# Performance work log

Hardware: AMD Instinct MI355X
Metric: run time of the kernel (lower is better)

The kernel has to match this reference:

```python
import jax, jax.numpy as jnp
import numpy as np

NEG_SLOPE = 0.01  # nn.LeakyReLU default


def gcn_conv(x, src, dst, deg_inv_sqrt, W, b, n_nodes):
    """PyG GCNConv with self-loops already folded into (src, dst, deg_inv_sqrt).
    out = scatter_add(norm_e * (x @ W)[src]) + b, norm_e = d_src^-1/2 * d_dst^-1/2."""
    h = x @ W  # [N, F_out] -- transform first (F_out < F_in saves gather traffic)
    norm = (deg_inv_sqrt[src] * deg_inv_sqrt[dst])[:, None]  # [E, 1]
    msg = h[src] * norm  # [E, F_out]
    return jax.ops.segment_sum(msg, dst, num_segments=n_nodes) + b


def setup_inputs() -> dict:
    key = jax.random.key(0)
    ks = jax.random.split(key, 8)
    N, E, F_IN, F_HID, F_OUT = 50000, 800000, 256, 128, 64
    x = jax.random.normal(ks[0], (N, F_IN), dtype=jnp.float32)
    edge_index = jax.random.randint(ks[1], (2, E), 0, N, dtype=jnp.int64)
    def glorot(k, shape):
        lim = float(np.sqrt(6.0 / (shape[0] + shape[1])))
        return jax.random.uniform(k, shape, jnp.float32, -lim, lim)
    return {
        "x": x,
        "edge_index": edge_index,
        "W1": glorot(ks[2], (F_IN, F_HID)),
        "b1": jnp.zeros((F_HID,), jnp.float32),
        "W_mu": glorot(ks[3], (F_HID, F_OUT)),
        "b_mu": jnp.zeros((F_OUT,), jnp.float32),
        "W_logvar": glorot(ks[4], (F_HID, F_OUT)),
        "b_logvar": jnp.zeros((F_OUT,), jnp.float32),
    }


def reference(x, edge_index, W1, b1, W_mu, b_mu, W_logvar, b_logvar):
    n_nodes = x.shape[0]
    loops = jnp.arange(n_nodes, dtype=edge_index.dtype)
    src = jnp.concatenate([edge_index[0], loops])
    dst = jnp.concatenate([edge_index[1], loops])
    # degree on destination nodes (includes self-loop); >= 1 so rsqrt is safe
    deg = jax.ops.segment_sum(jnp.ones_like(dst, dtype=x.dtype), dst, num_segments=n_nodes)
    deg_inv_sqrt = jax.lax.rsqrt(deg)

    h = gcn_conv(x, src, dst, deg_inv_sqrt, W1, b1, n_nodes)
    h = jax.nn.leaky_relu(h, NEG_SLOPE)
    mu = gcn_conv(h, src, dst, deg_inv_sqrt, W_mu, b_mu, n_nodes)
    logvar = gcn_conv(h, src, dst, deg_inv_sqrt, W_logvar, b_logvar, n_nodes)
    return (mu, logvar)
```

## Files before the change

### kernel.cpp

```cpp
#include <hip/hip_runtime.h>

#define NEG_SLOPE 0.01f
#define EPB 4096
#define NB_SHIFT 8

typedef __attribute__((ext_vector_type(8))) short bf16x8;
typedef __attribute__((ext_vector_type(4))) float floatx4;

__device__ __forceinline__ short f2bf(float f) {
    union { float f; unsigned u; } v; v.f = f;
    unsigned u = v.u;
    u += 0x7FFF + ((u >> 16) & 1);
    return (short)(u >> 16);
}
__device__ __forceinline__ float bf2f(short s) {
    union { unsigned u; float f; } v;
    v.u = ((unsigned)(unsigned short)s) << 16;
    return v.f;
}


__launch_bounds__(256)
__global__ void hist_pack(const int* __restrict__ dst, int E, int B, int K,
                          int* __restrict__ btot,
                          const float* __restrict__ W1, const float* __restrict__ Wmu,
                          const float* __restrict__ Wlv,
                          short* __restrict__ w1f, short* __restrict__ wcatf) {
    __shared__ int lh[256];
    int bid = blockIdx.x;
    int tid = threadIdx.x;
    if (bid < B) {
        lh[tid] = 0;
        __syncthreads();
        int lo = bid * EPB, hi = min(lo + EPB, E);
        for (int e = lo + tid; e < hi; e += 256)
            atomicAdd(&lh[dst[e] >> NB_SHIFT], 1);
        __syncthreads();
        int v = lh[tid];
        if (v) atomicAdd(&btot[tid], v);
    } else {
        int i = (bid - B) * 256 + tid;
        if (i < 128 * 256) {
            int j  = i & 7;
            int ln = (i >> 3) & 15;
            int q  = (i >> 7) & 3;
            int t  = (i >> 9) & 7;
            int kb = i >> 12;
            int n = t * 16 + ln;
            int k = kb * 32 + q * 8 + j;
            w1f[i] = f2bf(W1[k * 128 + n]);
        } else {
            int i2 = i - 128 * 256;
            int j  = i2 & 7;
            int ln = (i2 >> 3) & 15;
            int q  = (i2 >> 7) & 3;
            int t  = (i2 >> 9) & 7;
            int kb = i2 >> 12;
            int n = t * 16 + ln;
            int k = kb * 32 + q * 8 + j;
            wcatf[i2] = f2bf((n < 64) ? Wmu[k * 64 + n] : Wlv[k * 64 + (n - 64)]);
        }
    }
}

__global__ void bucket_scan(const int* __restrict__ btot, int K, int E,
                            int* __restrict__ bstart, int* __restrict__ bcur) {
    __shared__ int waveTot[4];
    __shared__ int waveOff[4];
    int tid = threadIdx.x;
    int lane = tid & 63, wave = tid >> 6;
    int v = (tid < K) ? btot[tid] : 0;
    int s = v;
    #pragma unroll
    for (int o = 1; o < 64; o <<= 1) {
        int t = __shfl_up(s, o);
        if (lane >= o) s += t;
    }
    if (lane == 63) waveTot[wave] = s;
    __syncthreads();
    if (tid == 0) {
        int acc = 0;
        #pragma unroll
        for (int w = 0; w < 4; w++) { waveOff[w] = acc; acc += waveTot[w]; }
    }
    __syncthreads();
    int excl = s - v + waveOff[wave];
    if (tid < K) { bstart[tid] = excl; bcur[tid] = excl; }
    if (tid == 0) bstart[K] = E;
}

template<int K>
__device__ __forceinline__ void gemm1_body(int blk, int tid, const float* __restrict__ Ap,
                                           const short* __restrict__ Bfrag,
                                           short* __restrict__ C, int M) {
    int w = tid >> 6;
    int lane = tid & 63;
    int ln = lane & 15;
    int q  = lane >> 4;
    int rowTile = blk * 128 + w * 32;

    int r0 = rowTile + ln;
    int r1 = rowTile + 16 + ln;
    int r0c = (r0 < M) ? r0 : (M - 1);
    int r1c = (r1 < M) ? r1 : (M - 1);

    const float* a0F = Ap + (size_t)r0c * K + q * 8;
    const float* a1F = Ap + (size_t)r1c * K + q * 8;
    const short* bLane = Bfrag + lane * 8;

    floatx4 acc[2][8];
    #pragma unroll
    for (int f = 0; f < 2; f++)
        #pragma unroll
        for (int t = 0; t < 8; t++) acc[f][t] = (floatx4){0.f, 0.f, 0.f, 0.f};

    constexpr int NIT = K / 32;
    #pragma unroll
    for (int kb = 0; kb < NIT; kb++) {
        int kt = kb * 32;
        bf16x8 aF0, aF1;
        float4 x0 = *(const float4*)(a0F + kt);
        float4 x1 = *(const float4*)(a0F + kt + 4);
        float4 y0 = *(const float4*)(a1F + kt);
        float4 y1 = *(const float4*)(a1F + kt + 4);
        aF0[0] = f2bf(x0.x); aF0[1] = f2bf(x0.y); aF0[2] = f2bf(x0.z); aF0[3] = f2bf(x0.w);
        aF0[4] = f2bf(x1.x); aF0[5] = f2bf(x1.y); aF0[6] = f2bf(x1.z); aF0[7] = f2bf(x1.w);
        aF1[0] = f2bf(y0.x); aF1[1] = f2bf(y0.y); aF1[2] = f2bf(y0.z); aF1[3] = f2bf(y0.w);
        aF1[4] = f2bf(y1.x); aF1[5] = f2bf(y1.y); aF1[6] = f2bf(y1.z); aF1[7] = f2bf(y1.w);
        bf16x8 bF[8];
        #pragma unroll
        for (int t = 0; t < 8; t++)
            bF[t] = *(const bf16x8*)(bLane + (size_t)(kb * 8 + t) * 512);
        #pragma unroll
        for (int t = 0; t < 8; t++) {
            acc[0][t] = __builtin_amdgcn_mfma_f32_16x16x32_bf16(aF0, bF[t], acc[0][t], 0, 0, 0);
            acc[1][t] = __builtin_amdgcn_mfma_f32_16x16x32_bf16(aF1, bF[t], acc[1][t], 0, 0, 0);
        }
    }

    #pragma unroll
    for (int f = 0; f < 2; f++) {
        #pragma unroll
        for (int reg = 0; reg < 4; reg++) {
            int r = rowTile + f * 16 + q * 4 + reg;
            if (r < M) {
                #pragma unroll
                for (int t = 0; t < 8; t++)
                    C[(size_t)r * 128 + t * 16 + ln] = f2bf(acc[f][t][reg]);
            }
        }
    }
}

__launch_bounds__(256)
__global__ void scatter_gemm1(const int* __restrict__ src, const int* __restrict__ dst,
                              int E, int B, int* __restrict__ bcur,
                              unsigned* __restrict__ bucketed,
                              const float* __restrict__ x, const short* __restrict__ w1f,
                              short* __restrict__ z1, int M) {
    __shared__ int lh[256];
    __shared__ int lofs[256];
    __shared__ int gbase[256];
    __shared__ unsigned srt[EPB];
    __shared__ int waveTot[4];
    __shared__ int waveOff[4];
    int bid = blockIdx.x;
    int tid = threadIdx.x;
    if (bid < B) {
        lh[tid] = 0;
        __syncthreads();
        int lo = bid * EPB, hi = min(lo + EPB, E);
        for (int e = lo + tid; e < hi; e += 256)
            atomicAdd(&lh[dst[e] >> NB_SHIFT], 1);
        __syncthreads();
        int v = lh[tid];
        int lane = tid & 63, wave = tid >> 6;
        int s = v;
        #pragma unroll
        for (int o = 1; o < 64; o <<= 1) {
            int t = __shfl_up(s, o);
            if (lane >= o) s += t;
        }
        if (lane == 63) waveTot[wave] = s;
        __syncthreads();
        if (tid == 0) {
            int acc = 0;
            #pragma unroll
            for (int w = 0; w < 4; w++) { waveOff[w] = acc; acc += waveTot[w]; }
        }
        __syncthreads();
        int excl = s - v + waveOff[wave];
        lofs[tid] = excl;
        if (v) gbase[tid] = atomicAdd(&bcur[tid], v);
        __syncthreads();
        lh[tid] = excl;
        __syncthreads();
        for (int e = lo + tid; e < hi; e += 256) {
            int d = dst[e];
            unsigned rec = (unsigned)(src[e] & 0xFFFF) | ((unsigned)d << 16);
            int p = atomicAdd(&lh[d >> NB_SHIFT], 1);
            srt[p] = rec;
        }
        __syncthreads();
        int cnt = hi - lo;
        for (int p = tid; p < cnt; p += 256) {
            unsigned r = srt[p];
            int k = r >> 24;
            bucketed[gbase[k] + (p - lofs[k])] = r;
        }
    } else {
        gemm1_body<256>(bid - B, tid, x, w1f, z1, M);
    }
}

__global__ void fill_csr_deg(const unsigned* __restrict__ bucketed,
                             const int* __restrict__ bstart,
                             int* __restrict__ row_ptr, int* __restrict__ row_end,
                             float* __restrict__ dis,
                             unsigned short* __restrict__ csr_src, int N) {
    __shared__ int cnt[256];
    __shared__ int rp[256];
    __shared__ int waveTot[4];
    __shared__ int waveOff[4];
    __shared__ unsigned short lcsr[8192];
    int k = blockIdx.x;
    int tid = threadIdx.x;
    int base = k << NB_SHIFT;
    cnt[tid] = 0;
    __syncthreads();
    int lo = bstart[k], hi = bstart[k + 1];
    int m = hi - lo;
    for (int e = lo + tid; e < hi; e += 256)
        atomicAdd(&cnt[(bucketed[e] >> 16) & 255], 1);
    __syncthreads();
    int v = cnt[tid];
    int lane = tid & 63, wave = tid >> 6;
    int s = v;
    #pragma unroll
    for (int o = 1; o < 64; o <<= 1) {
        int t = __shfl_up(s, o);
        if (lane >= o) s += t;
    }
    if (lane == 63) waveTot[wave] = s;
    __syncthreads();
    if (tid == 0) {
        int acc = 0;
        #pragma unroll
        for (int w = 0; w < 4; w++) { waveOff[w] = acc; acc += waveTot[w]; }
    }
    __syncthreads();
    int excl = s - v + waveOff[wave];
    rp[tid] = excl;
    int node = base + tid;
    if (node < N) {
        row_ptr[node] = lo + excl;
        row_end[node] = lo + excl + v;
        dis[node] = rsqrtf(1.0f + (float)v);
    }
    __syncthreads();
    if (m <= 8192) {
        for (int e = lo + tid; e < hi; e += 256) {
            unsigned sd = bucketed[e];
            int p = atomicAdd(&rp[(sd >> 16) & 255], 1);
            lcsr[p] = (unsigned short)(sd & 0xFFFFu);
        }
        __syncthreads();
        for (int i = tid; i < m; i += 256) csr_src[lo + i] = lcsr[i];
    } else {
        for (int e = lo + tid; e < hi; e += 256) {
            unsigned sd = bucketed[e];
            int p = atomicAdd(&rp[(sd >> 16) & 255], 1);
            csr_src[lo + p] = (unsigned short)(sd & 0xFFFFu);
        }
    }
}


__launch_bounds__(256)
__global__ void agg1_gemm2(const short* __restrict__ z1, const int* __restrict__ row_ptr,
                           const int* __restrict__ row_end,
                           const unsigned short* __restrict__ csr_src,
                           const float* __restrict__ dis, const float* __restrict__ b1,
                           const short* __restrict__ wcatf,
                           short* __restrict__ z2, int N) {
    __shared__ short htile[64 * 128];
    int tid = threadIdx.x;
    int w = tid >> 6;
    int lane = tid & 63;
    int qi = lane >> 4;
    int fl = lane & 15;
    int fo = fl * 8;
    int base = blockIdx.x * 64;

    const short* zb = z1 + fo;
    for (int i = 0; i < 16; ++i) {
        int local = w * 16 + i;
        int node = base + local;
        int swz = ((local & 7) * 8);
        short* hrow = &htile[(local * 128 + fo) ^ swz];
        if (node < N) {
            int start = row_ptr[node], end = row_end[node];
            float acc[8];
            #pragma unroll
            for (int t = 0; t < 8; t++) acc[t] = 0.f;
            for (int bse = start; bse < end; bse += 64) {
                int n = end - bse; n = (n > 64) ? 64 : n;
                int idx = (int)csr_src[bse + ((lane < n) ? lane : 0)];
                float dl = dis[idx];
                for (int j = 0; j < n; j += 8) {
                    int j0 = j + qi;
                    int j1 = j0 + 4;
                    int c0 = (j0 < n) ? j0 : 0;
                    int c1 = (j1 < n) ? j1 : 0;
                    int s0 = __shfl(idx, c0);
                    int s1 = __shfl(idx, c1);
                    float d0 = __shfl(dl, c0);
                    float d1 = __shfl(dl, c1);
                    if (j0 >= n) d0 = 0.f;
                    if (j1 >= n) d1 = 0.f;
                    bf16x8 zv0 = *(const bf16x8*)(zb + (size_t)s0 * 128);
                    bf16x8 zv1 = *(const bf16x8*)(zb + (size_t)s1 * 128);
                    #pragma unroll
                    for (int t = 0; t < 8; t++)
                        acc[t] = fmaf(d0, bf2f(zv0[t]), fmaf(d1, bf2f(zv1[t]), acc[t]));
                }
            }
            if (qi == 0) {
                float dn = dis[node];
                bf16x8 zs = *(const bf16x8*)(zb + (size_t)node * 128);
                #pragma unroll
                for (int t = 0; t < 8; t++) acc[t] = fmaf(dn, bf2f(zs[t]), acc[t]);
            }
            #pragma unroll
            for (int t = 0; t < 8; t++) {
                acc[t] += __shfl_xor(acc[t], 16);
                acc[t] += __shfl_xor(acc[t], 32);
            }
            if (qi == 0) {
                float d = dis[node];
                bf16x8 ov;
                #pragma unroll
                for (int t = 0; t < 8; t++) {
                    float v = fmaf(d, acc[t], b1[fo + t]);
                    v = (v > 0.f) ? v : NEG_SLOPE * v;
                    ov[t] = f2bf(v);
                }
                *(bf16x8*)hrow = ov;
            }
        } else if (qi == 0) {
            *(bf16x8*)hrow = (bf16x8){0, 0, 0, 0, 0, 0, 0, 0};
        }
    }
    __syncthreads();

    int rw = (w & 1) * 32;
    int tc = (w >> 1) * 4;
    int ln = fl;
    int q  = qi;
    int r0 = rw + ln;
    int r1 = rw + 16 + ln;
    const short* bLane = wcatf + lane * 8;

    floatx4 acc[2][4];
    #pragma unroll
    for (int f = 0; f < 2; f++)
        #pragma unroll
        for (int t = 0; t < 4; t++) acc[f][t] = (floatx4){0.f, 0.f, 0.f, 0.f};

    #pragma unroll
    for (int kb = 0; kb < 4; kb++) {
        int k0 = kb * 32 + q * 8;
        bf16x8 aF0 = *(const bf16x8*)&htile[(r0 * 128 + k0) ^ ((r0 & 7) * 8)];
        bf16x8 aF1 = *(const bf16x8*)&htile[(r1 * 128 + k0) ^ ((r1 & 7) * 8)];
        bf16x8 bF[4];
        #pragma unroll
        for (int t = 0; t < 4; t++)
            bF[t] = *(const bf16x8*)(bLane + (size_t)(kb * 8 + tc + t) * 512);
        #pragma unroll
        for (int t = 0; t < 4; t++) {
            acc[0][t] = __builtin_amdgcn_mfma_f32_16x16x32_bf16(aF0, bF[t], acc[0][t], 0, 0, 0);
            acc[1][t] = __builtin_amdgcn_mfma_f32_16x16x32_bf16(aF1, bF[t], acc[1][t], 0, 0, 0);
        }
    }

    #pragma unroll
    for (int f = 0; f < 2; f++) {
        #pragma unroll
        for (int reg = 0; reg < 4; reg++) {
            int gr = base + rw + f * 16 + q * 4 + reg;
            if (gr < N) {
                float s = dis[gr];
                #pragma unroll
                for (int t = 0; t < 4; t++)
                    z2[(size_t)gr * 128 + (tc + t) * 16 + ln] = f2bf(s * acc[f][t][reg]);
            }
        }
    }
}

__launch_bounds__(256)
__global__ void agg_layer2(const short* __restrict__ zp, const int* __restrict__ row_ptr,
                           const int* __restrict__ row_end,
                           const unsigned short* __restrict__ csr_src,
                           const float* __restrict__ dis, const float* __restrict__ b_mu,
                           const float* __restrict__ b_lv, float* __restrict__ out, int N) {
    int wave = threadIdx.x >> 6;
    int node = blockIdx.x * 4 + wave;
    if (node >= N) return;
    int lane = threadIdx.x & 63;
    int qi = lane >> 4;
    int fl = lane & 15;
    int fo = fl * 8;
    const short* zb = zp + fo;
    int start = row_ptr[node], end = row_end[node];
    float acc[8];
    #pragma unroll
    for (int t = 0; t < 8; t++) acc[t] = 0.f;
    for (int bse = start; bse < end; bse += 64) {
        int n = end - bse; n = (n > 64) ? 64 : n;
        int idx = (int)csr_src[bse + ((lane < n) ? lane : 0)];
        for (int j = 0; j < n; j += 8) {
            int j0 = j + qi;
            int j1 = j0 + 4;
            int c0 = (j0 < n) ? j0 : 0;
            int c1 = (j1 < n) ? j1 : 0;
            int s0 = __shfl(idx, c0);
            int s1 = __shfl(idx, c1);
            float w0 = (j0 < n) ? 1.f : 0.f;
            float w1 = (j1 < n) ? 1.f : 0.f;
            bf16x8 z0 = *(const bf16x8*)(zb + (size_t)s0 * 128);
            bf16x8 zv1 = *(const bf16x8*)(zb + (size_t)s1 * 128);
            #pragma unroll
            for (int t = 0; t < 8; t++)
                acc[t] = fmaf(w0, bf2f(z0[t]), fmaf(w1, bf2f(zv1[t]), acc[t]));
        }
    }
    if (qi == 0) {
        bf16x8 zs = *(const bf16x8*)(zb + (size_t)node * 128);
        #pragma unroll
        for (int t = 0; t < 8; t++) acc[t] += bf2f(zs[t]);
    }
    #pragma unroll
    for (int t = 0; t < 8; t++) {
        acc[t] += __shfl_xor(acc[t], 16);
        acc[t] += __shfl_xor(acc[t], 32);
    }
    if (qi == 0) {
        float d = dis[node];
        float r[8];
        if (fl < 8) {
            #pragma unroll
            for (int t = 0; t < 8; t++) r[t] = fmaf(d, acc[t], b_mu[fo + t]);
            float* p = out + (size_t)node * 64 + fo;
            *(float4*)p       = make_float4(r[0], r[1], r[2], r[3]);
            *(float4*)(p + 4) = make_float4(r[4], r[5], r[6], r[7]);
        } else {
            #pragma unroll
            for (int t = 0; t < 8; t++) r[t] = fmaf(d, acc[t], b_lv[fo - 64 + t]);
            float* p = out + (size_t)N * 64 + (size_t)node * 64 + (fo - 64);
            *(float4*)p       = make_float4(r[0], r[1], r[2], r[3]);
            *(float4*)(p + 4) = make_float4(r[4], r[5], r[6], r[7]);
        }
    }
}


extern "C" void kernel_launch(void* const* d_in, const int* in_sizes, int n_in,
                              void* d_out, int out_size, void* d_ws, size_t ws_size,
                              hipStream_t stream) {
    const float* x   = (const float*)d_in[0];
    const int*   ei  = (const int*)d_in[1];
    const float* W1  = (const float*)d_in[2];
    const float* b1  = (const float*)d_in[3];
    const float* Wmu = (const float*)d_in[4];
    const float* bmu = (const float*)d_in[5];
    const float* Wlv = (const float*)d_in[6];
    const float* blv = (const float*)d_in[7];
    float* out = (float*)d_out;

    const int F_IN = 256;
    int N = in_sizes[0] / F_IN;
    int E = in_sizes[1] / 2;
    const int* e_src = ei;
    const int* e_dst = ei + E;

    int B = (E + EPB - 1) / EPB;
    int K = (N + 255) >> NB_SHIFT;
    int Ggemm = (N + 127) / 128;
    int G2 = (N + 63) / 64;

    char* ws = (char*)d_ws;
    size_t off = 0;
    auto carve = [&](size_t bytes) -> void* {
        void* p = ws + off;
        off += (bytes + 255) & ~(size_t)255;
        return p;
    };
    int*      row_end  = (int*)   carve((size_t)N * 4);
    int*      row_ptr  = (int*)   carve((size_t)N * 4);
    float*    dis      = (float*) carve((size_t)N * 4);
    unsigned short* csr_src = (unsigned short*)carve((size_t)E * 2);
    short*    bufA     = (short*) carve((size_t)N * 128 * 2);
    short*    bufB     = (short*) carve((size_t)N * 128 * 2);
    short*    w1f      = (short*) carve(128 * 256 * 2);
    short*    wcatf    = (short*) carve(128 * 128 * 2);
    int*      bstart   = (int*)   carve((size_t)(K + 1) * 4);
    int*      bcur     = (int*)   carve((size_t)K * 4);
    int*      btot     = (int*)   carve((size_t)K * 4);
    unsigned* bucketed = (unsigned*)carve((size_t)E * 4);

    hipMemsetAsync(btot, 0, (size_t)K * 4, stream);
    hipLaunchKernelGGL(hist_pack, dim3(B + 192), dim3(256), 0, stream,
                       e_dst, E, B, K, btot, W1, Wmu, Wlv, w1f, wcatf);
    hipLaunchKernelGGL(bucket_scan, dim3(1), dim3(256), 0, stream, btot, K, E, bstart, bcur);
    hipLaunchKernelGGL(scatter_gemm1, dim3(B + Ggemm), dim3(256), 0, stream,
                       e_src, e_dst, E, B, bcur, bucketed, x, w1f, bufA, N);
    hipLaunchKernelGGL(fill_csr_deg, dim3(K), dim3(256), 0, stream,
                       bucketed, bstart, row_ptr, row_end, dis, csr_src, N);
    hipLaunchKernelGGL(agg1_gemm2, dim3(G2), dim3(256), 0, stream,
                       bufA, row_ptr, row_end, csr_src, dis, b1, wcatf, bufB, N);
    hipLaunchKernelGGL(agg_layer2, dim3((N + 3) / 4), dim3(256), 0, stream,
                       bufB, row_ptr, row_end, csr_src, dis, bmu, blv, out, N);
}
```

Before: 232.1 us.

## Shrink agg1_gemm2 tile to 16 nodes per block for more parallelism

The fused layer-1 aggregation plus layer-2 GEMM kernel now handles 16 nodes per block instead of 64. Each wave aggregates 4 nodes and then computes two 16-column MFMA tiles over one 16-row A fragment, and the grid grows fourfold. The aim is better load balance and occupancy, since smaller LDS tiles and shorter serial aggregation loops per wave mean less tail imbalance. In exchange, each weight fragment is reloaded by more blocks and each block does less MFMA reuse.

```diff
diff --git a/kernel.cpp b/kernel.cpp
--- a/kernel.cpp
+++ b/kernel.cpp
@@ -18,7 +18,6 @@
     v.u = ((unsigned)(unsigned short)s) << 16;
     return v.f;
 }
-
 
 __launch_bounds__(256)
 __global__ void hist_pack(const int* __restrict__ dst, int E, int B, int K,
@@ -283,18 +282,19 @@
                            const float* __restrict__ dis, const float* __restrict__ b1,
                            const short* __restrict__ wcatf,
                            short* __restrict__ z2, int N) {
-    __shared__ short htile[64 * 128];
+    __shared__ short htile[16 * 128];
     int tid = threadIdx.x;
     int w = tid >> 6;
     int lane = tid & 63;
     int qi = lane >> 4;
     int fl = lane & 15;
     int fo = fl * 8;
-    int base = blockIdx.x * 64;
+    int base = blockIdx.x * 16;
 
     const short* zb = z1 + fo;
-    for (int i = 0; i < 16; ++i) {
-        int local = w * 16 + i;
+    #pragma unroll 1
+    for (int i = 0; i < 4; ++i) {
+        int local = w * 4 + i;
         int node = base + local;
         int swz = ((local & 7) * 8);
         short* hrow = &htile[(local * 128 + fo) ^ swz];
@@ -353,47 +353,33 @@
     }
     __syncthreads();
 
-    int rw = (w & 1) * 32;
-    int tc = (w >> 1) * 4;
-    int ln = fl;
-    int q  = qi;
-    int r0 = rw + ln;
-    int r1 = rw + 16 + ln;
+    int r0 = fl;
     const short* bLane = wcatf + lane * 8;
 
-    floatx4 acc[2][4];
-    #pragma unroll
-    for (int f = 0; f < 2; f++)
-        #pragma unroll
-        for (int t = 0; t < 4; t++) acc[f][t] = (floatx4){0.f, 0.f, 0.f, 0.f};
+    floatx4 acc[2];
+    #pragma unroll
+    for (int t = 0; t < 2; t++) acc[t] = (floatx4){0.f, 0.f, 0.f, 0.f};
 
     #pragma unroll
     for (int kb = 0; kb < 4; kb++) {
-        int k0 = kb * 32 + q * 8;
-        bf16x8 aF0 = *(const bf16x8*)&htile[(r0 * 128 + k0) ^ ((r0 & 7) * 8)];
-        bf16x8 aF1 = *(const bf16x8*)&htile[(r1 * 128 + k0) ^ ((r1 & 7) * 8)];
-        bf16x8 bF[4];
-        #pragma unroll
-        for (int t = 0; t < 4; t++)
-            bF[t] = *(const bf16x8*)(bLane + (size_t)(kb * 8 + tc + t) * 512);
-        #pragma unroll
-        for (int t = 0; t < 4; t++) {
-            acc[0][t] = __builtin_amdgcn_mfma_f32_16x16x32_bf16(aF0, bF[t], acc[0][t], 0, 0, 0);
-            acc[1][t] = __builtin_amdgcn_mfma_f32_16x16x32_bf16(aF1, bF[t], acc[1][t], 0, 0, 0);
-        }
-    }
-
-    #pragma unroll
-    for (int f = 0; f < 2; f++) {
-        #pragma unroll
-        for (int reg = 0; reg < 4; reg++) {
-            int gr = base + rw + f * 16 + q * 4 + reg;
-            if (gr < N) {
-                float s = dis[gr];
-                #pragma unroll
-                for (int t = 0; t < 4; t++)
-                    z2[(size_t)gr * 128 + (tc + t) * 16 + ln] = f2bf(s * acc[f][t][reg]);
-            }
+        int k0 = kb * 32 + qi * 8;
+        bf16x8 aF = *(const bf16x8*)&htile[(r0 * 128 + k0) ^ ((r0 & 7) * 8)];
+        #pragma unroll
+        for (int t = 0; t < 2; t++) {
+            int tt = w * 2 + t;
+            bf16x8 bF = *(const bf16x8*)(bLane + (size_t)(kb * 8 + tt) * 512);
+            acc[t] = __builtin_amdgcn_mfma_f32_16x16x32_bf16(aF, bF, acc[t], 0, 0, 0);
+        }
+    }
+
+    #pragma unroll
+    for (int reg = 0; reg < 4; reg++) {
+        int gr = base + qi * 4 + reg;
+        if (gr < N) {
+            float s = dis[gr];
+            #pragma unroll
+            for (int t = 0; t < 2; t++)
+                z2[(size_t)gr * 128 + (w * 2 + t) * 16 + fl] = f2bf(s * acc[t][reg]);
         }
     }
 }
@@ -487,7 +473,7 @@
     int B = (E + EPB - 1) / EPB;
     int K = (N + 255) >> NB_SHIFT;
     int Ggemm = (N + 127) / 128;
-    int G2 = (N + 63) / 64;
+    int G2 = (N + 15) / 16;
 
     char* ws = (char*)d_ws;
     size_t off = 0;
```

Measured after the change: 212.9 us. -8.3%, faster.
